# Performance work log

Measured on AMD Instinct MI355X. Metric: run time of the kernel, lower is better.

Reference implementation:

```python
import jax, jax.numpy as jnp
import numpy as np

NF, D, H, HD, NL, FF = 5, 64, 8, 8, 2, 128   # features, d_model, heads, head_dim, layers, ffn
NQ, QL, NC = 8, 3, 3                          # qubits, quantum layers, classes


def pos_encoding(S, d):
    pos = np.arange(S, dtype=np.float32)[:, None]
    div = np.exp(np.arange(0, d, 2, dtype=np.float32) * (-np.log(10000.0) / d))
    pe = np.zeros((S, d), np.float32)
    pe[:, 0::2] = np.sin(pos * div)
    pe[:, 1::2] = np.cos(pos * div)
    return jnp.asarray(pe)


def layernorm(x, g, b, eps=1e-5):
    m = x.mean(-1, keepdims=True)
    v = ((x - m) ** 2).mean(-1, keepdims=True)
    return (x - m) * jax.lax.rsqrt(v + eps) * g + b


def apply1q(psi, U, w):
    # psi: (2,)*NQ complex state; apply 2x2 gate U on wire w
    p = jnp.moveaxis(psi, w, 0)
    sh = p.shape
    p = (U @ p.reshape(2, -1)).reshape(sh)
    return jnp.moveaxis(p, 0, w)


def cnot(psi, c, t):
    p = jnp.moveaxis(psi, (c, t), (0, 1))
    sh = p.shape
    p = p.reshape(2, 2, -1)
    p = jnp.stack([p[0], p[1, ::-1]], 0).reshape(sh)  # flip target when control=1
    return jnp.moveaxis(p, (0, 1), (c, t))


def rx_mat(t):
    c, s = jnp.cos(t / 2), jnp.sin(t / 2)
    return jnp.stack([jnp.stack([c + 0j, -1j * s]), jnp.stack([-1j * s, c + 0j])]).astype(jnp.complex64)


def rot_mat(phi, th, om):
    # qml.Rot = RZ(om) RY(th) RZ(phi)
    c, s = jnp.cos(th / 2), jnp.sin(th / 2)
    return jnp.stack([
        jnp.stack([jnp.exp(-0.5j * (phi + om)) * c, -jnp.exp(0.5j * (phi - om)) * s]),
        jnp.stack([jnp.exp(-0.5j * (phi - om)) * s, jnp.exp(0.5j * (phi + om)) * c]),
    ]).astype(jnp.complex64)


def quantum_circuit(angles, weights):
    # angles: [NQ], weights: [QL, NQ, 3]. Circuit: QL x (AngleEmbedding(RX) + StronglyEntanglingLayer(range=1))
    psi = jnp.zeros((2,) * NQ, jnp.complex64).at[(0,) * NQ].set(1.0)
    for l in range(QL):
        for w in range(NQ):
            psi = apply1q(psi, rx_mat(angles[w]), w)
        for w in range(NQ):
            psi = apply1q(psi, rot_mat(weights[l, w, 0], weights[l, w, 1], weights[l, w, 2]), w)
        for w in range(NQ):
            psi = cnot(psi, w, (w + 1) % NQ)
    prob = jnp.abs(psi) ** 2
    zs = []
    for w in range(NC):  # <Z_w> = p(0_w) - p(1_w)
        marg = prob.sum(axis=tuple(i for i in range(NQ) if i != w))
        zs.append(marg[0] - marg[1])
    # von Neumann entropy of wires 0..3 (trace out wires 4..7), natural log
    mat = psi.reshape(16, 16)
    rho = mat @ mat.conj().T
    ev = jnp.clip(jnp.linalg.eigvalsh(rho), 1e-10, 1.0)
    ent = -jnp.sum(ev * jnp.log(ev))
    return jnp.stack(zs), ent


def setup_inputs() -> dict:
    key = jax.random.key(0)
    ks = jax.random.split(key, 30)
    sc = 0.02
    inp = {
        'x': jax.random.normal(ks[0], (16, 1024, NF), jnp.float32),
        'Wemb': sc * jax.random.normal(ks[1], (NF, D)), 'bemb': jnp.zeros((D,)),
        'Wq': sc * jax.random.normal(ks[2], (NL, D, D)), 'bq': jnp.zeros((NL, D)),
        'Wk': sc * jax.random.normal(ks[3], (NL, D, D)), 'bk': jnp.zeros((NL, D)),
        'Wv': sc * jax.random.normal(ks[4], (NL, D, D)), 'bv': jnp.zeros((NL, D)),
        'Wo': sc * jax.random.normal(ks[5], (NL, D, D)), 'bo': jnp.zeros((NL, D)),
        'ln1g': jnp.ones((NL, D)), 'ln1b': jnp.zeros((NL, D)),
        'ln2g': jnp.ones((NL, D)), 'ln2b': jnp.zeros((NL, D)),
        'Wf1': sc * jax.random.normal(ks[6], (NL, D, FF)), 'bf1': jnp.zeros((NL, FF)),
        'Wf2': sc * jax.random.normal(ks[7], (NL, FF, D)), 'bf2': jnp.zeros((NL, D)),
        'Wp1': sc * jax.random.normal(ks[8], (D, 32)), 'bp1': jnp.zeros((32,)),
        'Wp2': sc * jax.random.normal(ks[9], (32, NQ)), 'bp2': jnp.zeros((NQ,)),
        'qweights': jax.random.normal(ks[10], (QL, NQ, 3)),
    }
    return inp


def reference(x, Wemb, bemb, Wq, bq, Wk, bk, Wv, bv, Wo, bo, ln1g, ln1b, ln2g, ln2b,
              Wf1, bf1, Wf2, bf2, Wp1, bp1, Wp2, bp2, qweights):
    B, S, _ = x.shape
    h = x @ Wemb + bemb + pos_encoding(S, D)[None]  # aug + dropout are identity in eval
    scale = np.float32(1.0 / np.sqrt(HD))
    for l in range(NL):
        q = (h @ Wq[l] + bq[l]).reshape(B, S, H, HD).transpose(0, 2, 1, 3)
        k = (h @ Wk[l] + bk[l]).reshape(B, S, H, HD).transpose(0, 2, 1, 3)
        v = (h @ Wv[l] + bv[l]).reshape(B, S, H, HD).transpose(0, 2, 1, 3)
        att = jax.nn.softmax(jnp.einsum('bhsd,bhtd->bhst', q, k) * scale, axis=-1)
        o = jnp.einsum('bhst,bhtd->bhsd', att, v).transpose(0, 2, 1, 3).reshape(B, S, D)
        h = layernorm(h + o @ Wo[l] + bo[l], ln1g[l], ln1b[l])
        ff = jax.nn.relu(h @ Wf1[l] + bf1[l]) @ Wf2[l] + bf2[l]
        h = layernorm(h + ff, ln2g[l], ln2b[l])
    pooled = h.mean(1)
    feats = jax.nn.relu(pooled @ Wp1 + bp1) @ Wp2 + bp2
    angles = jnp.tanh(feats) * np.float32(np.pi)
    logits, ent = jax.vmap(quantum_circuit, in_axes=(0, None))(angles, qweights)
    return logits, ent
```

## Files before the change

kernel.cpp:

```cpp
#include <hip/hip_runtime.h>
#include <math.h>

#define BB 16
#define SS 1024
#define NF 5
#define DD 64
#define HH 8
#define HDIM 8
#define NLAYER 2
#define FFD 128
#define NQ 8
#define QLAY 3
#define NC 3
#define NSWEEP 5
#define BHS_TOT (BB * HH * SS)

typedef __fp16 hf2 __attribute__((ext_vector_type(2)));
typedef __fp16 h8  __attribute__((ext_vector_type(8)));
typedef float  f4x __attribute__((ext_vector_type(4)));

__device__ __forceinline__ int   f2i_(float x) { union { float f; int i; } u; u.f = x; return u.i; }
__device__ __forceinline__ float i2f_(int x)   { union { float f; int i; } u; u.i = x; return u.f; }

__device__ __forceinline__ float bperm_(int pa, float x) {
    return i2f_(__builtin_amdgcn_ds_bpermute(pa, f2i_(x)));
}

__device__ __forceinline__ float half32_(float x) {
#if defined(__has_builtin)
#if __has_builtin(__builtin_amdgcn_permlane32_swap)
    int xi = f2i_(x);
    auto r = __builtin_amdgcn_permlane32_swap(xi, xi, false, false);
    int r0 = (int)r[0], r1 = (int)r[1];
    return i2f_(r0 == xi ? r1 : r0);
#else
    return __shfl_xor(x, 32);
#endif
#else
    return __shfl_xor(x, 32);
#endif
}

template<int M> __device__ __forceinline__ float lx(float x) {
    if constexpr (M == 0) {
        return x;
    } else if constexpr (M == 1) {
        return i2f_(__builtin_amdgcn_update_dpp(0, f2i_(x), 0xB1, 0xF, 0xF, true));
    } else if constexpr (M == 2) {
        return i2f_(__builtin_amdgcn_update_dpp(0, f2i_(x), 0x4E, 0xF, 0xF, true));
    } else if constexpr (M == 3) {
        return i2f_(__builtin_amdgcn_update_dpp(0, f2i_(x), 0x1B, 0xF, 0xF, true));
    } else if constexpr (M < 32) {
        return i2f_(__builtin_amdgcn_ds_swizzle(f2i_(x), (M << 10) | 0x1F));
    } else {
        return lx<M & 31>(half32_(x));
    }
}

__device__ __forceinline__ float wsum64_(float v) {
    v += lx<32>(v);
    v += lx<16>(v);
    v += lx<8>(v);
    v += lx<4>(v);
    v += lx<2>(v);
    v += lx<1>(v);
    return v;
}

__global__ __launch_bounds__(64) void k_qkv0(const float* __restrict__ x,
                                             const float* __restrict__ Wemb,
                                             const float* __restrict__ bemb,
                                             const float* __restrict__ Wq, const float* __restrict__ bq,
                                             const float* __restrict__ Wk, const float* __restrict__ bk,
                                             const float* __restrict__ Wv, const float* __restrict__ bv,
                                             hf2* __restrict__ qh, hf2* __restrict__ kh,
                                             hf2* __restrict__ vt, float* __restrict__ h) {
    __shared__ float hrow[4][DD];
    int d   = threadIdx.x;
    int bs0 = blockIdx.x * 4;
    {
        int i = d >> 1;
        float div = expf((float)(2 * i) * (-9.210340371976184f / 64.0f));
#pragma unroll
        for (int r = 0; r < 4; ++r) {
            int bs = bs0 + r;
            int s  = bs & (SS - 1);
            const float* xr = x + bs * NF;
            float acc = bemb[d];
#pragma unroll
            for (int f = 0; f < NF; ++f) acc += xr[f] * Wemb[f * DD + d];
            float ang = (float)s * div;
            float pe = (d & 1) ? cosf(ang) : sinf(ang);
            float hv = acc + pe;
            hrow[r][d] = hv;
            h[bs * DD + d] = hv;
        }
    }
    __syncthreads();
    const float* wq = Wq;
    const float* wk = Wk;
    const float* wv = Wv;
    float aq[4], ak[4], av[4];
    float bqv = bq[d], bkv = bk[d], bvv = bv[d];
#pragma unroll
    for (int r = 0; r < 4; ++r) { aq[r] = bqv; ak[r] = bkv; av[r] = bvv; }
#pragma unroll 4
    for (int i = 0; i < DD; ++i) {
        float wqv = wq[i * DD + d], wkv = wk[i * DD + d], wvv = wv[i * DD + d];
#pragma unroll
        for (int r = 0; r < 4; ++r) {
            float hv = hrow[r][i];
            aq[r] += hv * wqv; ak[r] += hv * wkv; av[r] += hv * wvv;
        }
    }
    int hh = d >> 3, hd = d & 7;
    const float qs = 0.3535533906f;
    float aqp[4], akp[4];
#pragma unroll
    for (int r = 0; r < 4; ++r) { aqp[r] = lx<1>(aq[r]); akp[r] = lx<1>(ak[r]); }
    if ((hd & 1) == 0) {
#pragma unroll
        for (int r = 0; r < 4; ++r) {
            int bs = bs0 + r;
            int b = bs >> 10, s = bs & 1023;
            int bhs = ((b * HH + hh) << 10) | s;
            qh[bhs * 4 + (hd >> 1)] = __builtin_amdgcn_cvt_pkrtz(aq[r] * qs, aqp[r] * qs);
            kh[bhs * 4 + (hd >> 1)] = __builtin_amdgcn_cvt_pkrtz(ak[r], akp[r]);
        }
    }
    {
        int b = bs0 >> 10, s0 = bs0 & 1023;
        int vrow = (b * HH + hh) * 8 + hd;
        hf2* vp = vt + vrow * 512 + (s0 >> 1);
        vp[0] = __builtin_amdgcn_cvt_pkrtz(av[0], av[1]);
        vp[1] = __builtin_amdgcn_cvt_pkrtz(av[2], av[3]);
    }
}

__global__ __launch_bounds__(256) void k_attn(const float4* __restrict__ qh4,
                                              const float4* __restrict__ kh4,
                                              const float4* __restrict__ vt4,
                                              float* __restrict__ Ao) {
    int bh  = blockIdx.x;
    int sb  = blockIdx.y;
    int tid = threadIdx.x;
    int wv  = tid >> 6;
    int L   = tid & 63;
    int m = L & 15, quad = L >> 4;
    union U { float4 f; h8 h; };
    h8 hz = {0,0,0,0,0,0,0,0};
    h8 bQ = hz;
    if (quad == 0) { U u; u.f = qh4[(bh << 10) | (sb * 64 + wv * 16 + m)]; bQ = u.h; }
    int kmap = 8 * (m >> 2) + (m & 3);
    const float4* kbase = kh4 + (bh << 10);
    const float4* vbase = vt4 + ((bh * 8 + (m & 7)) << 7);
    f4x Oacc = {0.f, 0.f, 0.f, 0.f};
    float ls = 0.f;
    for (int kc = 0; kc < 32; ++kc) {
        h8 aK0 = hz, aK1 = hz;
        if (quad == 0) {
            U u0, u1;
            u0.f = kbase[kc * 32 + kmap];
            u1.f = kbase[kc * 32 + kmap + 4];
            aK0 = u0.h; aK1 = u1.h;
        }
        f4x S0 = {0.f,0.f,0.f,0.f}, S1 = {0.f,0.f,0.f,0.f};
        S0 = __builtin_amdgcn_mfma_f32_16x16x32_f16(aK0, bQ, S0, 0, 0, 0);
        S1 = __builtin_amdgcn_mfma_f32_16x16x32_f16(aK1, bQ, S1, 0, 0, 0);
        float p0 = __expf(S0[0]), p1 = __expf(S0[1]);
        float p2 = __expf(S0[2]), p3 = __expf(S0[3]);
        float p4 = __expf(S1[0]), p5 = __expf(S1[1]);
        float p6 = __expf(S1[2]), p7 = __expf(S1[3]);
        ls += (p0 + p1 + p2 + p3) + (p4 + p5 + p6 + p7);
        hf2 c0 = __builtin_amdgcn_cvt_pkrtz(p0, p1);
        hf2 c1 = __builtin_amdgcn_cvt_pkrtz(p2, p3);
        hf2 c2 = __builtin_amdgcn_cvt_pkrtz(p4, p5);
        hf2 c3 = __builtin_amdgcn_cvt_pkrtz(p6, p7);
        h8 aP;
        aP[0] = c0[0]; aP[1] = c0[1]; aP[2] = c1[0]; aP[3] = c1[1];
        aP[4] = c2[0]; aP[5] = c2[1]; aP[6] = c3[0]; aP[7] = c3[1];
        h8 bV = hz;
        if (m < 8) {
            U uv; uv.f = vbase[kc * 4 + quad];
            bV = uv.h;
        }
        Oacc = __builtin_amdgcn_mfma_f32_16x16x32_f16(aP, bV, Oacc, 0, 0, 0);
    }
    ls += lx<16>(ls);
    ls += lx<32>(ls);
    float d0 = bperm_((4 * quad + 0) << 2, ls);
    float d1 = bperm_((4 * quad + 1) << 2, ls);
    float d2 = bperm_((4 * quad + 2) << 2, ls);
    float d3 = bperm_((4 * quad + 3) << 2, ls);
    if (m < 8) {
        int srow = sb * 64 + wv * 16 + quad * 4;
        int base = (((bh << 10) | srow) << 3) + m;
        Ao[base]      = Oacc[0] / d0;
        Ao[base + 8]  = Oacc[1] / d1;
        Ao[base + 16] = Oacc[2] / d2;
        Ao[base + 24] = Oacc[3] / d3;
    }
}

__global__ __launch_bounds__(128) void k_mid(const float* __restrict__ Ao,
                                             const float* __restrict__ Wo, const float* __restrict__ bo,
                                             const float* __restrict__ g1, const float* __restrict__ b1,
                                             const float* __restrict__ Wf1, const float* __restrict__ bf1,
                                             const float* __restrict__ Wf2, const float* __restrict__ bf2,
                                             const float* __restrict__ g2, const float* __restrict__ b2,
                                             float* __restrict__ h, int l, int fuse,
                                             const float* __restrict__ Wq, const float* __restrict__ bq,
                                             const float* __restrict__ Wk, const float* __restrict__ bk,
                                             const float* __restrict__ Wv, const float* __restrict__ bv,
                                             hf2* __restrict__ qh, hf2* __restrict__ kh,
                                             hf2* __restrict__ vt) {
    __shared__ float orow[4][DD];
    __shared__ float h1s[4][DD];
    __shared__ float frow[4][FFD];
    __shared__ float hfin[4][DD];
    int t    = threadIdx.x;
    int d    = t & 63;
    int half = t >> 6;
    int bs0  = blockIdx.x * 4;
    int hh = d >> 3, hd = d & 7;
    int r0 = half * 2, r1 = r0 + 1;

#pragma unroll
    for (int rr = 0; rr < 2; ++rr) {
        int r  = r0 + rr;
        int bs = bs0 + r;
        int b = bs >> 10, s = bs & 1023;
        int bhs = ((b * HH + hh) << 10) | s;
        orow[r][d] = Ao[(bhs << 3) + hd];
    }
    __syncthreads();

    {
        const float* w = Wo + l * DD * DD;
        float bias = bo[l * DD + d];
        float acc0 = bias, acc1 = bias;
#pragma unroll 4
        for (int i = 0; i < DD; ++i) {
            float wv = w[i * DD + d];
            acc0 += orow[r0][i] * wv;
            acc1 += orow[r1][i] * wv;
        }
        float gg = g1[l * DD + d], bb = b1[l * DD + d];
        float accs[2] = {acc0, acc1};
#pragma unroll
        for (int rr = 0; rr < 2; ++rr) {
            int r = r0 + rr;
            float a = accs[rr] + h[(bs0 + r) * DD + d];
            float sum = wsum64_(a);
            float mean = sum * (1.f / 64.f);
            float dx = a - mean;
            float vs = wsum64_(dx * dx);
            float rstd = rsqrtf(vs * (1.f / 64.f) + 1e-5f);
            h1s[r][d] = dx * rstd * gg + bb;
        }
    }
    __syncthreads();

    {
        const float* w = Wf1 + l * DD * FFD;
        float bv_ = bf1[l * FFD + t];
        float a0 = bv_, a1 = bv_, a2 = bv_, a3 = bv_;
#pragma unroll 4
        for (int i = 0; i < DD; ++i) {
            float wv = w[i * FFD + t];
            a0 += h1s[0][i]*wv; a1 += h1s[1][i]*wv;
            a2 += h1s[2][i]*wv; a3 += h1s[3][i]*wv;
        }
        frow[0][t] = fmaxf(a0, 0.f); frow[1][t] = fmaxf(a1, 0.f);
        frow[2][t] = fmaxf(a2, 0.f); frow[3][t] = fmaxf(a3, 0.f);
    }
    __syncthreads();

    {
        const float* w = Wf2 + l * FFD * DD;
        float bias = bf2[l * DD + d];
        float acc0 = bias, acc1 = bias;
#pragma unroll 4
        for (int i = 0; i < FFD; ++i) {
            float wv = w[i * DD + d];
            acc0 += frow[r0][i] * wv;
            acc1 += frow[r1][i] * wv;
        }
        float gg = g2[l * DD + d], bb = b2[l * DD + d];
        float accs[2] = {acc0, acc1};
#pragma unroll
        for (int rr = 0; rr < 2; ++rr) {
            int r = r0 + rr;
            float a = accs[rr] + h1s[r][d];
            float sum = wsum64_(a);
            float mean = sum * (1.f / 64.f);
            float dx = a - mean;
            float vs = wsum64_(dx * dx);
            float rstd = rsqrtf(vs * (1.f / 64.f) + 1e-5f);
            float hv = dx * rstd * gg + bb;
            hfin[r][d] = hv;
            h[(bs0 + r) * DD + d] = hv;
        }
    }

    if (!fuse) return;

    __syncthreads();
    const int l1 = l + 1;
    if (t < 64) {
        const float* wq = Wq + l1 * DD * DD;
        const float* wk = Wk + l1 * DD * DD;
        float aq[4], ak[4];
        float bqv = bq[l1 * DD + d], bkv = bk[l1 * DD + d];
#pragma unroll
        for (int r = 0; r < 4; ++r) { aq[r] = bqv; ak[r] = bkv; }
#pragma unroll 4
        for (int i = 0; i < DD; ++i) {
            float wqv = wq[i * DD + d], wkv = wk[i * DD + d];
#pragma unroll
            for (int r = 0; r < 4; ++r) {
                float hv = hfin[r][i];
                aq[r] += hv * wqv; ak[r] += hv * wkv;
            }
        }
        const float qs = 0.3535533906f;
        float aqp[4], akp[4];
#pragma unroll
        for (int r = 0; r < 4; ++r) { aqp[r] = lx<1>(aq[r]); akp[r] = lx<1>(ak[r]); }
        if ((hd & 1) == 0) {
#pragma unroll
            for (int r = 0; r < 4; ++r) {
                int bs = bs0 + r;
                int b = bs >> 10, s = bs & 1023;
                int bhs = ((b * HH + hh) << 10) | s;
                qh[bhs * 4 + (hd >> 1)] = __builtin_amdgcn_cvt_pkrtz(aq[r] * qs, aqp[r] * qs);
                kh[bhs * 4 + (hd >> 1)] = __builtin_amdgcn_cvt_pkrtz(ak[r], akp[r]);
            }
        }
    } else {
        const float* wv = Wv + l1 * DD * DD;
        float av[4];
        float bvv = bv[l1 * DD + d];
#pragma unroll
        for (int r = 0; r < 4; ++r) av[r] = bvv;
#pragma unroll 4
        for (int i = 0; i < DD; ++i) {
            float wvv = wv[i * DD + d];
#pragma unroll
            for (int r = 0; r < 4; ++r) av[r] += hfin[r][i] * wvv;
        }
        int b = bs0 >> 10, s0 = bs0 & 1023;
        int vrow = (b * HH + hh) * 8 + hd;
        hf2* vp = vt + vrow * 512 + (s0 >> 1);
        vp[0] = __builtin_amdgcn_cvt_pkrtz(av[0], av[1]);
        vp[1] = __builtin_amdgcn_cvt_pkrtz(av[2], av[3]);
    }
}

__global__ __launch_bounds__(256) void k_tail(const float* __restrict__ h,
                                              const float* __restrict__ Wp1, const float* __restrict__ bp1,
                                              const float* __restrict__ Wp2, const float* __restrict__ bp2,
                                              const float* __restrict__ qw,
                                              float* __restrict__ out) {
    __shared__ float part[4][DD];
    __shared__ float pool_s[DD];
    __shared__ float hid[32];
    __shared__ float ang_s[NQ];
    __shared__ float ucoef[QLAY * 16][8];
    __shared__ float2 Ps2[256];
    int b = blockIdx.x; int t = threadIdx.x;
    int L = t;
    int lb4 = (t & 63) << 2;

    {
        int d = t & 63, ch = t >> 6;
        const float* hp = h + (b * SS + ch * 256) * DD + d;
        float acc = 0.f;
#pragma unroll 8
        for (int s = 0; s < 256; ++s) acc += hp[s * DD];
        part[ch][d] = acc;
    }
    __syncthreads();
    if (t < 64) pool_s[t] = (part[0][t] + part[1][t] + part[2][t] + part[3][t]) * (1.f / 1024.f);
    __syncthreads();
    if (t < 32) {
        float a = bp1[t];
#pragma unroll 8
        for (int i = 0; i < DD; ++i) a += pool_s[i] * Wp1[i * 32 + t];
        hid[t] = fmaxf(a, 0.f);
    }
    __syncthreads();
    if (t < NQ) {
        float a = bp2[t];
#pragma unroll 8
        for (int j = 0; j < 32; ++j) a += hid[j] * Wp2[j * NQ + t];
        ang_s[t] = tanhf(a) * 3.14159265358979f;
    }
    __syncthreads();

    if (t < QLAY * 16) {
        int l = t >> 4, g8 = t & 15, w = g8 & 7;
        float u00r, u00i, u01r, u01i, u10r, u10i, u11r, u11i;
        if (g8 < 8) {
            float ha = 0.5f * ang_s[w];
            float c = __cosf(ha), s = __sinf(ha);
            u00r = c;   u00i = 0.f; u01r = 0.f; u01i = -s;
            u10r = 0.f; u10i = -s;  u11r = c;   u11i = 0.f;
        } else {
            const float* p3 = qw + (l * NQ + w) * 3;
            float phi = p3[0], th = p3[1], om = p3[2];
            float ct = __cosf(0.5f * th), st = __sinf(0.5f * th);
            float al = 0.5f * (phi + om), be = 0.5f * (phi - om);
            float ca = __cosf(al), sa = __sinf(al), cb = __cosf(be), sb = __sinf(be);
            u00r =  ct * ca; u00i = -ct * sa;
            u01r = -st * cb; u01i = -st * sb;
            u10r =  st * cb; u10i = -st * sb;
            u11r =  ct * ca; u11i =  ct * sa;
        }
        float* up = ucoef[t];
        up[0] = u00r; up[1] = u00i; up[2] = u01r; up[3] = u01i;
        up[4] = u10r; up[5] = u10i; up[6] = u11r; up[7] = u11i;
    }
    __syncthreads();

    float ar[4], ai[4];
#pragma unroll
    for (int r = 0; r < 4; ++r) { ar[r] = 0.f; ai[r] = 0.f; }
    if (L == 0) ar[0] = 1.f;

    if (t < 64) {
#pragma unroll 1
        for (int l = 0; l < QLAY; ++l) {
#pragma unroll 1
            for (int g8 = 0; g8 < 16; ++g8) {
                const float* up = ucoef[(l << 4) | g8];
                float u00r = up[0], u00i = up[1], u01r = up[2], u01i = up[3];
                float u10r = up[4], u10i = up[5], u11r = up[6], u11i = up[7];
                int p = 7 - (g8 & 7);
                if (p >= 6) {
#pragma unroll
                    for (int pi_ = 0; pi_ < 2; ++pi_) {
                        int lo = (p == 7) ? pi_ : pi_ * 2;
                        int hi = (p == 7) ? pi_ + 2 : pi_ * 2 + 1;
                        float r0 = ar[lo], m0 = ai[lo], r1 = ar[hi], m1 = ai[hi];
                        ar[lo] = u00r*r0 - u00i*m0 + u01r*r1 - u01i*m1;
                        ai[lo] = u00r*m0 + u00i*r0 + u01r*m1 + u01i*r1;
                        ar[hi] = u10r*r0 - u10i*m0 + u11r*r1 - u11i*m1;
                        ai[hi] = u10r*m0 + u10i*r0 + u11r*m1 + u11i*r1;
                    }
                } else {
                    int pa  = lb4 ^ (4 << p);
                    int bit = (L >> p) & 1;
                    float car = bit ? u11r : u00r, cai = bit ? u11i : u00i;
                    float cpr = bit ? u10r : u01r, cpi = bit ? u10i : u01i;
#pragma unroll
                    for (int r = 0; r < 4; ++r) {
                        float pre = bperm_(pa, ar[r]);
                        float pim = bperm_(pa, ai[r]);
                        float nr = car*ar[r] - cai*ai[r] + cpr*pre - cpi*pim;
                        float ni = car*ai[r] + cai*ar[r] + cpr*pim + cpi*pre;
                        ar[r] = nr; ai[r] = ni;
                    }
                }
            }
            { float t0=ar[2]; ar[2]=ar[3]; ar[3]=t0; t0=ai[2]; ai[2]=ai[3]; ai[3]=t0; }
            ar[1] = half32_(ar[1]); ai[1] = half32_(ai[1]);
            ar[3] = half32_(ar[3]); ai[3] = half32_(ai[3]);
#pragma unroll 1
            for (int w = 2; w <= 6; ++w) {
                int pc = 7 - w, pt = 6 - w;
                int pa = lb4 ^ (4 << pt);
                bool ctrl = (L >> pc) & 1;
#pragma unroll
                for (int r = 0; r < 4; ++r) {
                    float swr = bperm_(pa, ar[r]);
                    float swi = bperm_(pa, ai[r]);
                    ar[r] = ctrl ? swr : ar[r];
                    ai[r] = ctrl ? swi : ai[r];
                }
            }
            {
                bool ctrl = L & 1;
                float n0r = ctrl ? ar[2] : ar[0], n2r = ctrl ? ar[0] : ar[2];
                float n0i = ctrl ? ai[2] : ai[0], n2i = ctrl ? ai[0] : ai[2];
                float n1r = ctrl ? ar[3] : ar[1], n3r = ctrl ? ar[1] : ar[3];
                float n1i = ctrl ? ai[3] : ai[1], n3i = ctrl ? ai[1] : ai[3];
                ar[0]=n0r; ar[1]=n1r; ar[2]=n2r; ar[3]=n3r;
                ai[0]=n0i; ai[1]=n1i; ai[2]=n2i; ai[3]=n3i;
            }
        }

        {
            float p0 = ar[0]*ar[0]+ai[0]*ai[0];
            float p1 = ar[1]*ar[1]+ai[1]*ai[1];
            float p2 = ar[2]*ar[2]+ai[2]*ai[2];
            float p3 = ar[3]*ar[3]+ai[3]*ai[3];
            float z0 = p0 + p1 - p2 - p3;
            float z1 = p0 - p1 + p2 - p3;
            float zs = p0 + p1 + p2 + p3;
            float z2 = (L & 32) ? -zs : zs;
#pragma unroll 1
            for (int off = 1; off < 64; off <<= 1) {
                int pa = lb4 ^ (off << 2);
                z0 += bperm_(pa, z0);
                z1 += bperm_(pa, z1);
                z2 += bperm_(pa, z2);
            }
            if (L == 0) {
                out[b * NC + 0] = z0;
                out[b * NC + 1] = z1;
                out[b * NC + 2] = z2;
            }
        }

#pragma unroll
        for (int r = 0; r < 4; ++r) Ps2[(r << 6) | L] = make_float2(ar[r], ai[r]);
    }
    __syncthreads();

    if (t < 64) {
        int c   = L >> 2;
        int seg = L & 3;
        float gr[4], gi[4];
#pragma unroll
        for (int j = 0; j < 4; ++j) {
            float2 tv = Ps2[(seg * 4 + j) * 16 + c];
            gr[j] = tv.x; gi[j] = tv.y;
        }
        float alm = 0.f;
#pragma unroll
        for (int j = 0; j < 4; ++j) alm += gr[j]*gr[j] + gi[j]*gi[j];
        alm += lx<1>(alm);
        alm += lx<2>(alm);

#pragma unroll 1
        for (int sweep = 0; sweep < NSWEEP; ++sweep) {
#pragma unroll 1
            for (int m = 1; m <= 15; ++m) {
                int pa = lb4 ^ (m << 4);
                float pgr[4], pgi[4];
#pragma unroll
                for (int j = 0; j < 4; ++j) {
                    pgr[j] = bperm_(pa, gr[j]);
                    pgi[j] = bperm_(pa, gi[j]);
                }
                float bep = bperm_(pa, alm);
                float d = 0.f, e = 0.f;
#pragma unroll
                for (int j = 0; j < 4; ++j) {
                    d += gr[j]*pgr[j] + gi[j]*pgi[j];
                    e += gr[j]*pgi[j] - gi[j]*pgr[j];
                }
                d += lx<1>(d); e += lx<1>(e);
                d += lx<2>(d); e += lx<2>(e);
                float g2 = d*d + e*e;
                float cth = 1.f, sth = 0.f, cph = 1.f, sph = 0.f, gn = 0.f;
                if (g2 > 1e-26f) {
                    gn = __builtin_amdgcn_sqrtf(g2);
                    float ginv = __builtin_amdgcn_rcpf(gn);
                    cph = d * ginv; sph = -e * ginv;
                    float tau = (alm - bep) * (0.5f * ginv);
                    float tt = ((tau >= 0.f) ? 1.f : -1.f) *
                               __builtin_amdgcn_rcpf(fabsf(tau) + __builtin_amdgcn_sqrtf(1.f + tau*tau));
                    cth = __builtin_amdgcn_rsqf(1.f + tt*tt);
                    sth = tt * cth;
                }
#pragma unroll
                for (int j = 0; j < 4; ++j) {
                    float er = cph*pgr[j] - sph*pgi[j];
                    float ei = cph*pgi[j] + sph*pgr[j];
                    gr[j] = cth * gr[j] + sth * er;
                    gi[j] = cth * gi[j] + sth * ei;
                }
                alm = cth*cth*alm + sth*sth*bep + 2.f*cth*sth*gn;
            }
        }

        float alm2 = 0.f;
#pragma unroll
        for (int j = 0; j < 4; ++j) alm2 += gr[j]*gr[j] + gi[j]*gi[j];
        alm2 += lx<1>(alm2);
        alm2 += lx<2>(alm2);

        float ev = fminf(fmaxf(alm2, 1e-10f), 1.0f);
        float term = -ev * __logf(ev);
#pragma unroll 1
        for (int off = 4; off < 64; off <<= 1) term += bperm_(lb4 ^ (off << 2), term);
        if (L == 0) out[BB * NC + b] = term;
    }
}

extern "C" void kernel_launch(void* const* d_in, const int* in_sizes, int n_in,
                              void* d_out, int out_size, void* d_ws, size_t ws_size,
                              hipStream_t stream) {
    const float* x    = (const float*)d_in[0];
    const float* Wemb = (const float*)d_in[1];
    const float* bemb = (const float*)d_in[2];
    const float* Wq   = (const float*)d_in[3];
    const float* bq   = (const float*)d_in[4];
    const float* Wk   = (const float*)d_in[5];
    const float* bk   = (const float*)d_in[6];
    const float* Wv   = (const float*)d_in[7];
    const float* bv   = (const float*)d_in[8];
    const float* Wo   = (const float*)d_in[9];
    const float* bo   = (const float*)d_in[10];
    const float* ln1g = (const float*)d_in[11];
    const float* ln1b = (const float*)d_in[12];
    const float* ln2g = (const float*)d_in[13];
    const float* ln2b = (const float*)d_in[14];
    const float* Wf1  = (const float*)d_in[15];
    const float* bf1  = (const float*)d_in[16];
    const float* Wf2  = (const float*)d_in[17];
    const float* bf2  = (const float*)d_in[18];
    const float* Wp1  = (const float*)d_in[19];
    const float* bp1  = (const float*)d_in[20];
    const float* Wp2  = (const float*)d_in[21];
    const float* bp2  = (const float*)d_in[22];
    const float* qwts = (const float*)d_in[23];
    float* out = (float*)d_out;

    const size_t M = 1u << 20;
    float* ws   = (float*)d_ws;
    float* h    = ws;
    hf2*   qh   = (hf2*)(ws + M);
    hf2*   kh   = (hf2*)(ws + M + M / 2);
    hf2*   vt   = (hf2*)(ws + 2 * M);
    float* Ao   = ws + 2 * M + M / 2;

    k_qkv0<<<BB * SS / 4, 64, 0, stream>>>(x, Wemb, bemb, Wq, bq, Wk, bk, Wv, bv,
                                           qh, kh, vt, h);
    k_attn<<<dim3(BB * HH, 16), 256, 0, stream>>>((const float4*)qh, (const float4*)kh,
                                                  (const float4*)vt, Ao);
    k_mid<<<BB * SS / 4, 128, 0, stream>>>(Ao, Wo, bo, ln1g, ln1b,
                                           Wf1, bf1, Wf2, bf2, ln2g, ln2b, h, 0, 1,
                                           Wq, bq, Wk, bk, Wv, bv, qh, kh, vt);
    k_attn<<<dim3(BB * HH, 16), 256, 0, stream>>>((const float4*)qh, (const float4*)kh,
                                                  (const float4*)vt, Ao);
    k_mid<<<BB * SS / 4, 128, 0, stream>>>(Ao, Wo, bo, ln1g, ln1b,
                                           Wf1, bf1, Wf2, bf2, ln2g, ln2b, h, 1, 0,
                                           Wq, bq, Wk, bk, Wv, bv, qh, kh, vt);
    k_tail<<<BB, 256, 0, stream>>>(h, Wp1, bp1, Wp2, bp2, qwts, out);
}
```

Baseline: 287.7 us.

## Use exp2 softmax, permlane/DPP shuffles, and fuse mean-pool partials into final layer

Folds log2(e) into the query scale so attention can use the hardware exp2 instruction in place of expf. Replaces ds_bpermute lane exchanges in the reductions and quantum-state updates with DPP, swizzle and permlane swap primitives, and unrolls those shuffle loops. The last transformer layer now writes per-block partial row sums, so the tail kernel sums 64 partials instead of 256 rows per chunk. The Jacobi rotation angle is computed by a different closed form. These cut shuffle latency and tail reads, at the cost of slightly different numerics in the eigenvalue step.

```diff
diff --git a/kernel.cpp b/kernel.cpp
--- a/kernel.cpp
+++ b/kernel.cpp
@@ -13,7 +13,6 @@
 #define QLAY 3
 #define NC 3
 #define NSWEEP 5
-#define BHS_TOT (BB * HH * SS)
 
 typedef __fp16 hf2 __attribute__((ext_vector_type(2)));
 typedef __fp16 h8  __attribute__((ext_vector_type(8)));
@@ -57,15 +56,42 @@
     }
 }
 
+__device__ __forceinline__ float half16_(float x) {
+#if defined(__has_builtin)
+#if __has_builtin(__builtin_amdgcn_permlane16_swap)
+    int xi = f2i_(x);
+    auto r = __builtin_amdgcn_permlane16_swap(xi, xi, false, false);
+    int r0 = (int)r[0], r1 = (int)r[1];
+    return i2f_(r0 == xi ? r1 : r0);
+#else
+    return lx<16>(x);
+#endif
+#else
+    return lx<16>(x);
+#endif
+}
+
 __device__ __forceinline__ float wsum64_(float v) {
-    v += lx<32>(v);
-    v += lx<16>(v);
+    v += half32_(v);
+    v += half16_(v);
     v += lx<8>(v);
     v += lx<4>(v);
     v += lx<2>(v);
     v += lx<1>(v);
     return v;
 }
+
+#if defined(__has_builtin)
+#if __has_builtin(__builtin_amdgcn_exp2f)
+#define EXP2F(x) __builtin_amdgcn_exp2f(x)
+#else
+#define EXP2F(x) exp2f(x)
+#endif
+#else
+#define EXP2F(x) exp2f(x)
+#endif
+
+#define QSCALE (0.3535533906f * 1.4426950408889634f)
 
 __global__ __launch_bounds__(64) void k_qkv0(const float* __restrict__ x,
                                              const float* __restrict__ Wemb,
@@ -114,7 +140,7 @@
         }
     }
     int hh = d >> 3, hd = d & 7;
-    const float qs = 0.3535533906f;
+    const float qs = QSCALE;
     float aqp[4], akp[4];
 #pragma unroll
     for (int r = 0; r < 4; ++r) { aqp[r] = lx<1>(aq[r]); akp[r] = lx<1>(ak[r]); }
@@ -167,10 +193,10 @@
         f4x S0 = {0.f,0.f,0.f,0.f}, S1 = {0.f,0.f,0.f,0.f};
         S0 = __builtin_amdgcn_mfma_f32_16x16x32_f16(aK0, bQ, S0, 0, 0, 0);
         S1 = __builtin_amdgcn_mfma_f32_16x16x32_f16(aK1, bQ, S1, 0, 0, 0);
-        float p0 = __expf(S0[0]), p1 = __expf(S0[1]);
-        float p2 = __expf(S0[2]), p3 = __expf(S0[3]);
-        float p4 = __expf(S1[0]), p5 = __expf(S1[1]);
-        float p6 = __expf(S1[2]), p7 = __expf(S1[3]);
+        float p0 = EXP2F(S0[0]), p1 = EXP2F(S0[1]);
+        float p2 = EXP2F(S0[2]), p3 = EXP2F(S0[3]);
+        float p4 = EXP2F(S1[0]), p5 = EXP2F(S1[1]);
+        float p6 = EXP2F(S1[2]), p7 = EXP2F(S1[3]);
         ls += (p0 + p1 + p2 + p3) + (p4 + p5 + p6 + p7);
         hf2 c0 = __builtin_amdgcn_cvt_pkrtz(p0, p1);
         hf2 c1 = __builtin_amdgcn_cvt_pkrtz(p2, p3);
@@ -186,8 +212,8 @@
         }
         Oacc = __builtin_amdgcn_mfma_f32_16x16x32_f16(aP, bV, Oacc, 0, 0, 0);
     }
-    ls += lx<16>(ls);
-    ls += lx<32>(ls);
+    ls += half16_(ls);
+    ls += half32_(ls);
     float d0 = bperm_((4 * quad + 0) << 2, ls);
     float d1 = bperm_((4 * quad + 1) << 2, ls);
     float d2 = bperm_((4 * quad + 2) << 2, ls);
@@ -213,7 +239,7 @@
                                              const float* __restrict__ Wk, const float* __restrict__ bk,
                                              const float* __restrict__ Wv, const float* __restrict__ bv,
                                              hf2* __restrict__ qh, hf2* __restrict__ kh,
-                                             hf2* __restrict__ vt) {
+                                             hf2* __restrict__ vt, float* __restrict__ pp2) {
     __shared__ float orow[4][DD];
     __shared__ float h1s[4][DD];
     __shared__ float frow[4][FFD];
@@ -303,7 +329,13 @@
         }
     }
 
-    if (!fuse) return;
+    if (!fuse) {
+        __syncthreads();
+        if (t < 64) {
+            pp2[blockIdx.x * DD + t] = (hfin[0][t] + hfin[1][t]) + (hfin[2][t] + hfin[3][t]);
+        }
+        return;
+    }
 
     __syncthreads();
     const int l1 = l + 1;
@@ -323,7 +355,7 @@
                 aq[r] += hv * wqv; ak[r] += hv * wkv;
             }
         }
-        const float qs = 0.3535533906f;
+        const float qs = QSCALE;
         float aqp[4], akp[4];
 #pragma unroll
         for (int r = 0; r < 4; ++r) { aqp[r] = lx<1>(aq[r]); akp[r] = lx<1>(ak[r]); }
@@ -357,7 +389,7 @@
     }
 }
 
-__global__ __launch_bounds__(256) void k_tail(const float* __restrict__ h,
+__global__ __launch_bounds__(256) void k_tail(const float* __restrict__ pp2,
                                               const float* __restrict__ Wp1, const float* __restrict__ bp1,
                                               const float* __restrict__ Wp2, const float* __restrict__ bp2,
                                               const float* __restrict__ qw,
@@ -374,10 +406,10 @@
 
     {
         int d = t & 63, ch = t >> 6;
-        const float* hp = h + (b * SS + ch * 256) * DD + d;
+        const float* pp = pp2 + (b * 256 + ch * 64) * DD + d;
         float acc = 0.f;
 #pragma unroll 8
-        for (int s = 0; s < 256; ++s) acc += hp[s * DD];
+        for (int j = 0; j < 64; ++j) acc += pp[j * DD];
         part[ch][d] = acc;
     }
     __syncthreads();
@@ -449,16 +481,33 @@
                         ai[hi] = u10r*m0 + u10i*r0 + u11r*m1 + u11i*r1;
                     }
                 } else {
-                    int pa  = lb4 ^ (4 << p);
                     int bit = (L >> p) & 1;
                     float car = bit ? u11r : u00r, cai = bit ? u11i : u00i;
                     float cpr = bit ? u10r : u01r, cpi = bit ? u10i : u01i;
+                    float pre[4], pim[4];
+                    if (p == 5) {
+#pragma unroll
+                        for (int r = 0; r < 4; ++r) { pre[r] = half32_(ar[r]); pim[r] = half32_(ai[r]); }
+                    } else if (p == 4) {
+#pragma unroll
+                        for (int r = 0; r < 4; ++r) { pre[r] = half16_(ar[r]); pim[r] = half16_(ai[r]); }
+                    } else if (p == 3) {
+#pragma unroll
+                        for (int r = 0; r < 4; ++r) { pre[r] = lx<8>(ar[r]); pim[r] = lx<8>(ai[r]); }
+                    } else if (p == 2) {
+#pragma unroll
+                        for (int r = 0; r < 4; ++r) { pre[r] = lx<4>(ar[r]); pim[r] = lx<4>(ai[r]); }
+                    } else if (p == 1) {
+#pragma unroll
+                        for (int r = 0; r < 4; ++r) { pre[r] = lx<2>(ar[r]); pim[r] = lx<2>(ai[r]); }
+                    } else {
+#pragma unroll
+                        for (int r = 0; r < 4; ++r) { pre[r] = lx<1>(ar[r]); pim[r] = lx<1>(ai[r]); }
+                    }
 #pragma unroll
                     for (int r = 0; r < 4; ++r) {
-                        float pre = bperm_(pa, ar[r]);
-                        float pim = bperm_(pa, ai[r]);
-                        float nr = car*ar[r] - cai*ai[r] + cpr*pre - cpi*pim;
-                        float ni = car*ai[r] + cai*ar[r] + cpr*pim + cpi*pre;
+                        float nr = car*ar[r] - cai*ai[r] + cpr*pre[r] - cpi*pim[r];
+                        float ni = car*ai[r] + cai*ar[r] + cpr*pim[r] + cpi*pre[r];
                         ar[r] = nr; ai[r] = ni;
                     }
                 }
@@ -469,14 +518,28 @@
 #pragma unroll 1
             for (int w = 2; w <= 6; ++w) {
                 int pc = 7 - w, pt = 6 - w;
-                int pa = lb4 ^ (4 << pt);
                 bool ctrl = (L >> pc) & 1;
+                float swr[4], swi[4];
+                if (pt == 4) {
+#pragma unroll
+                    for (int r = 0; r < 4; ++r) { swr[r] = half16_(ar[r]); swi[r] = half16_(ai[r]); }
+                } else if (pt == 3) {
+#pragma unroll
+                    for (int r = 0; r < 4; ++r) { swr[r] = lx<8>(ar[r]); swi[r] = lx<8>(ai[r]); }
+                } else if (pt == 2) {
+#pragma unroll
+                    for (int r = 0; r < 4; ++r) { swr[r] = lx<4>(ar[r]); swi[r] = lx<4>(ai[r]); }
+                } else if (pt == 1) {
+#pragma unroll
+                    for (int r = 0; r < 4; ++r) { swr[r] = lx<2>(ar[r]); swi[r] = lx<2>(ai[r]); }
+                } else {
+#pragma unroll
+                    for (int r = 0; r < 4; ++r) { swr[r] = lx<1>(ar[r]); swi[r] = lx<1>(ai[r]); }
+                }
 #pragma unroll
                 for (int r = 0; r < 4; ++r) {
-                    float swr = bperm_(pa, ar[r]);
-                    float swi = bperm_(pa, ai[r]);
-                    ar[r] = ctrl ? swr : ar[r];
-                    ai[r] = ctrl ? swi : ai[r];
+                    ar[r] = ctrl ? swr[r] : ar[r];
+                    ai[r] = ctrl ? swi[r] : ai[r];
                 }
             }
             {
@@ -499,13 +562,12 @@
             float z1 = p0 - p1 + p2 - p3;
             float zs = p0 + p1 + p2 + p3;
             float z2 = (L & 32) ? -zs : zs;
-#pragma unroll 1
-            for (int off = 1; off < 64; off <<= 1) {
-                int pa = lb4 ^ (off << 2);
-                z0 += bperm_(pa, z0);
-                z1 += bperm_(pa, z1);
-                z2 += bperm_(pa, z2);
-            }
+            z0 += lx<1>(z0);   z1 += lx<1>(z1);   z2 += lx<1>(z2);
+            z0 += lx<2>(z0);   z1 += lx<2>(z1);   z2 += lx<2>(z2);
+            z0 += lx<4>(z0);   z1 += lx<4>(z1);   z2 += lx<4>(z2);
+            z0 += lx<8>(z0);   z1 += lx<8>(z1);   z2 += lx<8>(z2);
+            z0 += half16_(z0); z1 += half16_(z1); z2 += half16_(z2);
+            z0 += half32_(z0); z1 += half32_(z1); z2 += half32_(z2);
             if (L == 0) {
                 out[b * NC + 0] = z0;
                 out[b * NC + 1] = z1;
@@ -537,14 +599,34 @@
         for (int sweep = 0; sweep < NSWEEP; ++sweep) {
 #pragma unroll 1
             for (int m = 1; m <= 15; ++m) {
-                int pa = lb4 ^ (m << 4);
-                float pgr[4], pgi[4];
-#pragma unroll
-                for (int j = 0; j < 4; ++j) {
-                    pgr[j] = bperm_(pa, gr[j]);
-                    pgi[j] = bperm_(pa, gi[j]);
+                int xm = m << 2;
+                float pgr[4], pgi[4], bep;
+                if ((xm & 12) == 0) {
+                    if (xm == 16) {
+#pragma unroll
+                        for (int j = 0; j < 4; ++j) { pgr[j] = half16_(gr[j]); pgi[j] = half16_(gi[j]); }
+                        bep = half16_(alm);
+                    } else if (xm == 32) {
+#pragma unroll
+                        for (int j = 0; j < 4; ++j) { pgr[j] = half32_(gr[j]); pgi[j] = half32_(gi[j]); }
+                        bep = half32_(alm);
+                    } else {
+#pragma unroll
+                        for (int j = 0; j < 4; ++j) {
+                            pgr[j] = half16_(half32_(gr[j]));
+                            pgi[j] = half16_(half32_(gi[j]));
+                        }
+                        bep = half16_(half32_(alm));
+                    }
+                } else {
+                    int pa = lb4 ^ (xm << 2);
+#pragma unroll
+                    for (int j = 0; j < 4; ++j) {
+                        pgr[j] = bperm_(pa, gr[j]);
+                        pgi[j] = bperm_(pa, gi[j]);
+                    }
+                    bep = bperm_(pa, alm);
                 }
-                float bep = bperm_(pa, alm);
                 float d = 0.f, e = 0.f;
 #pragma unroll
                 for (int j = 0; j < 4; ++j) {
@@ -560,10 +642,10 @@
                     float ginv = __builtin_amdgcn_rcpf(gn);
                     cph = d * ginv; sph = -e * ginv;
                     float tau = (alm - bep) * (0.5f * ginv);
-                    float tt = ((tau >= 0.f) ? 1.f : -1.f) *
-                               __builtin_amdgcn_rcpf(fabsf(tau) + __builtin_amdgcn_sqrtf(1.f + tau*tau));
-                    cth = __builtin_amdgcn_rsqf(1.f + tt*tt);
-                    sth = tt * cth;
+                    float rr = __builtin_amdgcn_rsqf(1.f + tau*tau);
+                    float co = fminf(fabsf(tau) * rr, 1.0f);
+                    cth = __builtin_amdgcn_sqrtf(0.5f + 0.5f*co);
+                    sth = copysignf(__builtin_amdgcn_sqrtf(0.5f - 0.5f*co), tau);
                 }
 #pragma unroll
                 for (int j = 0; j < 4; ++j) {
@@ -584,8 +666,10 @@
 
         float ev = fminf(fmaxf(alm2, 1e-10f), 1.0f);
         float term = -ev * __logf(ev);
-#pragma unroll 1
-        for (int off = 4; off < 64; off <<= 1) term += bperm_(lb4 ^ (off << 2), term);
+        term += lx<4>(term);
+        term += lx<8>(term);
+        term += half16_(term);
+        term += half32_(term);
         if (L == 0) out[BB * NC + b] = term;
     }
 }
@@ -626,6 +710,7 @@
     hf2*   kh   = (hf2*)(ws + M + M / 2);
     hf2*   vt   = (hf2*)(ws + 2 * M);
     float* Ao   = ws + 2 * M + M / 2;
+    float* pp2  = ws + 3 * M + M / 2;
 
     k_qkv0<<<BB * SS / 4, 64, 0, stream>>>(x, Wemb, bemb, Wq, bq, Wk, bk, Wv, bv,
                                            qh, kh, vt, h);
@@ -633,11 +718,11 @@
                                                   (const float4*)vt, Ao);
     k_mid<<<BB * SS / 4, 128, 0, stream>>>(Ao, Wo, bo, ln1g, ln1b,
                                            Wf1, bf1, Wf2, bf2, ln2g, ln2b, h, 0, 1,
-                                           Wq, bq, Wk, bk, Wv, bv, qh, kh, vt);
+                                           Wq, bq, Wk, bk, Wv, bv, qh, kh, vt, pp2);
     k_attn<<<dim3(BB * HH, 16), 256, 0, stream>>>((const float4*)qh, (const float4*)kh,
                                                   (const float4*)vt, Ao);
     k_mid<<<BB * SS / 4, 128, 0, stream>>>(Ao, Wo, bo, ln1g, ln1b,
                                            Wf1, bf1, Wf2, bf2, ln2g, ln2b, h, 1, 0,
-                                           Wq, bq, Wk, bk, Wv, bv, qh, kh, vt);
-    k_tail<<<BB, 256, 0, stream>>>(h, Wp1, bp1, Wp2, bp2, qwts, out);
-}
+                                           Wq, bq, Wk, bk, Wv, bv, qh, kh, vt, pp2);
+    k_tail<<<BB, 256, 0, stream>>>(pp2, Wp1, bp1, Wp2, bp2, qwts, out);
+}
```

New measurement: 292.4 us. No clear change (+1.6%).
